# Kernel optimization log

Hardware: AMD Instinct MI355X
Metric: run time of the kernel (lower is better)

Reference implementation:

```python
import jax, jax.numpy as jnp
import numpy as np

RES = (512, 512)
NUM_CLASSES = 80
LEVELS = [(8, 0.0, 64.0), (16, 64.0, 128.0), (32, 128.0, 256.0),
          (64, 256.0, 512.0), (128, 512.0, jnp.inf)]


def _encode(boxes, labels, box_valid):
    """Vectorized FCOS encode. boxes:[B,N,4] (x1,y1,x2,y2), labels:[B,N] int,
    box_valid:[B,N] nonzero=valid. Returns 15 channel-first grids:
    (cls_P3..P7, centerness_P3..P7, ltrb_P3..P7)."""
    H, W = RES
    B, N, _ = boxes.shape
    valid = box_valid != 0
    x1, y1, x2, y2 = boxes[..., 0], boxes[..., 1], boxes[..., 2], boxes[..., 3]
    areas = (x2 - x1) * (y2 - y1)
    # sort descending by area (torch.sort descending); invalid boxes last
    order = jnp.argsort(-jnp.where(valid, areas, -jnp.inf), axis=1)  # [B,N]
    sb = jnp.take_along_axis(boxes, order[..., None], axis=1)        # [B,N,4]
    sl = jnp.take_along_axis(labels, order, axis=1)                  # [B,N]
    sv = jnp.take_along_axis(valid, order, axis=1)                   # [B,N]

    # initial per-level grids (NHWC during the scan, like the torch code)
    state = []
    for s, _, _ in LEVELS:
        Hl, Wl = H // s, W // s
        state.append((jnp.zeros((B, Hl, Wl, NUM_CLASSES), jnp.float32),
                      jnp.zeros((B, Hl, Wl, 1), jnp.float32),
                      jnp.zeros((B, Hl, Wl, 4), jnp.float32)))
    state = tuple(state)

    cls_ids = jnp.arange(NUM_CLASSES)

    def step(st, xs):
        box, lab, vld = xs  # [B,4], [B], [B]
        bxmin, bymin, bxmax, bymax = box[:, 0], box[:, 1], box[:, 2], box[:, 3]
        onehot = lab[:, None] == cls_ids[None, :]  # [B,C] bool
        new_st = []
        for li, (s, rmin, rmax) in enumerate(LEVELS):
            Hl, Wl = H // s, W // s
            # int() truncation as in torch _find_box_positions
            xf = jnp.trunc(bxmin / s + 0.5)
            xl = jnp.trunc(bxmax / s - 0.5)
            yf = jnp.trunc(bymin / s + 0.5)
            yl = jnp.trunc(bymax / s - 0.5)
            ys = jnp.arange(Hl, dtype=jnp.float32)
            xg = jnp.arange(Wl, dtype=jnp.float32)
            my = (ys[None, :] >= yf[:, None]) & (ys[None, :] <= yl[:, None])  # [B,Hl]
            mx = (xg[None, :] >= xf[:, None]) & (xg[None, :] <= xl[:, None])  # [B,Wl]
            mask = my[:, :, None] & mx[:, None, :] & vld[:, None, None]       # [B,Hl,Wl]
            cy = (ys + 0.5) * s  # [Hl]
            cx = (xg + 0.5) * s  # [Wl]
            l_ = jnp.broadcast_to(cx[None, None, :] - bxmin[:, None, None], (B, Hl, Wl))
            t_ = jnp.broadcast_to(cy[None, :, None] - bymin[:, None, None], (B, Hl, Wl))
            r_ = jnp.broadcast_to(bxmax[:, None, None] - cx[None, None, :], (B, Hl, Wl))
            b_ = jnp.broadcast_to(bymax[:, None, None] - cy[None, :, None], (B, Hl, Wl))
            ltrb = jnp.stack([l_, t_, r_, b_], axis=-1)  # [B,Hl,Wl,4]
            num = jnp.minimum(l_, r_) * jnp.minimum(t_, b_)
            den = jnp.maximum(l_, r_) * jnp.maximum(t_, b_)
            cent = jnp.sqrt(jnp.clip(num / jnp.maximum(den, 1e-12), 1e-12))
            mval = jnp.max(ltrb, axis=-1)
            cond = mask & (mval >= rmin) & (mval < rmax)  # [B,Hl,Wl]
            cls, cen, bx = st[li]
            cls = jnp.where(mask[..., None] & onehot[:, None, None, :],
                            cond[..., None].astype(cls.dtype), cls)
            cen = jnp.where(mask[..., None], cent[..., None], cen)
            bx = jnp.where(cond[..., None], ltrb, bx)
            new_st.append((cls, cen, bx))
        return tuple(new_st), None

    xs = (jnp.transpose(sb, (1, 0, 2)), jnp.transpose(sl, (1, 0)),
          jnp.transpose(sv, (1, 0)))
    state, _ = jax.lax.scan(step, state, xs)

    # channel-first like the torch permute at the end
    to_cf = lambda a: jnp.transpose(a, (0, 3, 1, 2))
    cls_out = tuple(to_cf(st[0]) for st in state)
    cen_out = tuple(to_cf(st[1]) for st in state)
    box_out = tuple(to_cf(st[2]) for st in state)
    return cls_out + cen_out + box_out


def setup_inputs() -> dict:
    key = jax.random.key(0)
    k1, k2, k3, k4 = jax.random.split(key, 4)
    B, N = 32, 100
    ctr = jax.random.uniform(k1, (B, N, 2), minval=16.0, maxval=496.0)
    wh = jax.random.uniform(k2, (B, N, 2), minval=8.0, maxval=300.0)
    mins = jnp.clip(ctr - wh / 2, 0.0, 511.0)
    maxs = jnp.clip(ctr + wh / 2, 0.0, 511.0)
    boxes = jnp.concatenate([mins, maxs], axis=-1)  # [B,N,4] x1,y1,x2,y2
    labels = jax.random.randint(k3, (B, N), 0, NUM_CLASSES)
    box_valid = jax.random.randint(k4, (B, N), 0, 2)
    return {"boxes": boxes, "labels": labels, "box_valid": box_valid}


def reference(boxes, labels, box_valid):
    return _encode(boxes, labels, box_valid)
```

## Files before the change

### kernel.cpp

```cpp
#include <hip/hip_runtime.h>
#include <math.h>

#define NBOX 100
#define NBATCH 32
#define NCLS 80
#define PIX_PER_BATCH 5456

__global__ __launch_bounds__(128) void fcos_sort_kernel(
    const float* __restrict__ boxes,
    const int* __restrict__ labels,
    const int* __restrict__ valid,
    float4* __restrict__ sboxes,
    int* __restrict__ slab)
{
    int b = blockIdx.x;
    int tid = threadIdx.x;
    __shared__ float area_s[NBOX];
    __shared__ float4 box_s[NBOX];
    __shared__ int lab_s[NBOX];
    if (tid < NBOX) {
        float4 bx = ((const float4*)boxes)[b * NBOX + tid];
        int v = valid[b * NBOX + tid];
        float area = (bx.z - bx.x) * (bx.w - bx.y);
        area_s[tid] = (v != 0) ? area : -INFINITY;
        box_s[tid] = bx;
        lab_s[tid] = (v != 0) ? labels[b * NBOX + tid] : -1;
    }
    __syncthreads();
    if (tid < NBOX) {
        float my = area_s[tid];
        int rank = 0;
        #pragma unroll 4
        for (int j = 0; j < NBOX; ++j) {
            float aj = area_s[j];
            rank += ((aj > my) || (aj == my && j < tid)) ? 1 : 0;
        }
        sboxes[b * NBOX + rank] = box_s[tid];
        slab[b * NBOX + rank] = lab_s[tid];
    }
}

__global__ __launch_bounds__(256) void fcos_encode_kernel(
    const float4* __restrict__ sboxes,
    const int* __restrict__ slab,
    float* __restrict__ out)
{
    __shared__ float4 sb[NBOX];
    __shared__ int sl[NBOX];
    int b = blockIdx.y;
    int tid = threadIdx.x;
    if (tid < NBOX) {
        sb[tid] = sboxes[b * NBOX + tid];
        sl[tid] = slab[b * NBOX + tid];
    }
    __syncthreads();

    int p = blockIdx.x * 256 + tid;
    if (p >= PIX_PER_BATCH) return;

    int base, lw;
    float s, rmin, rmax;
    int coff, ceoff, boff;
    if (p < 4096)       { base = 0;    lw = 6; s = 8.f;   rmin = 0.f;   rmax = 64.f;
                          coff = 0;        ceoff = 13967360; boff = 14141952; }
    else if (p < 5120)  { base = 4096; lw = 5; s = 16.f;  rmin = 64.f;  rmax = 128.f;
                          coff = 10485760; ceoff = 14098432; boff = 14666240; }
    else if (p < 5376)  { base = 5120; lw = 4; s = 32.f;  rmin = 128.f; rmax = 256.f;
                          coff = 13107200; ceoff = 14131200; boff = 14797312; }
    else if (p < 5440)  { base = 5376; lw = 3; s = 64.f;  rmin = 256.f; rmax = 512.f;
                          coff = 13762560; ceoff = 14139392; boff = 14830080; }
    else                { base = 5440; lw = 2; s = 128.f; rmin = 512.f; rmax = INFINITY;
                          coff = 13926400; ceoff = 14141440; boff = 14838272; }

    int rel = p - base;
    int W = 1 << lw;
    int A = W * W;
    int y = rel >> lw;
    int x = rel & (W - 1);

    float xF = (float)x, yF = (float)y;
    float cxp = (xF + 0.5f) * s;
    float cyp = (yF + 0.5f) * s;
    float inv_s = 1.0f / s;

    unsigned long long bits_lo = 0ull;
    unsigned int bits_hi = 0u;
    float cen = 0.f;
    float bl = 0.f, bt = 0.f, br = 0.f, bb = 0.f;

    for (int i = 0; i < NBOX; ++i) {
        int lab = sl[i];
        if (lab < 0) continue;
        float4 bx4 = sb[i];
        float xf = truncf(bx4.x * inv_s + 0.5f);
        float xl = truncf(bx4.z * inv_s - 0.5f);
        float yf = truncf(bx4.y * inv_s + 0.5f);
        float yl = truncf(bx4.w * inv_s - 0.5f);
        bool mask = (yF >= yf) & (yF <= yl) & (xF >= xf) & (xF <= xl);
        if (!mask) continue;

        float l_ = cxp - bx4.x;
        float t_ = cyp - bx4.y;
        float r_ = bx4.z - cxp;
        float b_ = bx4.w - cyp;
        float num = fminf(l_, r_) * fminf(t_, b_);
        float den = fmaxf(l_, r_) * fmaxf(t_, b_);
        cen = sqrtf(fmaxf(num / fmaxf(den, 1e-12f), 1e-12f));
        float mval = fmaxf(fmaxf(l_, t_), fmaxf(r_, b_));
        bool ok = (mval >= rmin) & (mval < rmax);

        if (lab < 64) {
            unsigned long long bit = 1ull << lab;
            bits_lo = ok ? (bits_lo | bit) : (bits_lo & ~bit);
        } else {
            unsigned int bit = 1u << (lab - 64);
            bits_hi = ok ? (bits_hi | bit) : (bits_hi & ~bit);
        }
        if (ok) { bl = l_; bt = t_; br = r_; bb = b_; }
    }

    {
        size_t o = (size_t)coff + (size_t)b * NCLS * A + rel;
        #pragma unroll 8
        for (int c = 0; c < 64; ++c) {
            out[o + (size_t)c * A] = ((bits_lo >> c) & 1ull) ? 1.0f : 0.0f;
        }
        #pragma unroll 8
        for (int c = 0; c < 16; ++c) {
            out[o + (size_t)(64 + c) * A] = ((bits_hi >> c) & 1u) ? 1.0f : 0.0f;
        }
    }
    out[(size_t)ceoff + (size_t)b * A + rel] = cen;
    {
        size_t o = (size_t)boff + (size_t)b * 4 * A + rel;
        out[o] = bl;
        out[o + (size_t)A] = bt;
        out[o + (size_t)2 * A] = br;
        out[o + (size_t)3 * A] = bb;
    }
}

extern "C" void kernel_launch(void* const* d_in, const int* in_sizes, int n_in,
                              void* d_out, int out_size, void* d_ws, size_t ws_size,
                              hipStream_t stream) {
    const float* boxes = (const float*)d_in[0];
    const int* labels = (const int*)d_in[1];
    const int* valid = (const int*)d_in[2];
    float* out = (float*)d_out;

    float4* sboxes = (float4*)d_ws;
    int* slab = (int*)((char*)d_ws + NBATCH * NBOX * sizeof(float4));

    fcos_sort_kernel<<<NBATCH, 128, 0, stream>>>(boxes, labels, valid, sboxes, slab);

    dim3 grid((PIX_PER_BATCH + 255) / 256, NBATCH);
    fcos_encode_kernel<<<grid, 256, 0, stream>>>(sboxes, slab, out);
}
```

Before: 99.67 us.

## Fuse sort into encode kernel and vectorize output stores via shared staging

Removes the separate sort kernel by having every encode block redo the per-batch rank sort in shared memory, saving a launch and the workspace round-trip. The per-box loop now breaks at the first invalid box, since invalid boxes sort last. Per-pixel results are staged in shared memory and written as float4 stores, with each wavefront covering a subset of class channels. The cost is redundant sorting in each block, extra shared memory, and a second barrier.

```diff
diff --git a/kernel.cpp b/kernel.cpp
--- a/kernel.cpp
+++ b/kernel.cpp
@@ -6,153 +6,174 @@
 #define NCLS 80
 #define PIX_PER_BATCH 5456
 
-__global__ __launch_bounds__(128) void fcos_sort_kernel(
-    const float* __restrict__ boxes,
+__device__ __forceinline__ void level_of(int p, int& base, int& lw, float& s,
+                                         float& rmin, float& rmax,
+                                         int& coff, int& ceoff, int& boff) {
+    if (p < 4096)      { base=0;    lw=6; s=8.f;   rmin=0.f;   rmax=64.f;
+                         coff=0;        ceoff=13967360; boff=14141952; }
+    else if (p < 5120) { base=4096; lw=5; s=16.f;  rmin=64.f;  rmax=128.f;
+                         coff=10485760; ceoff=14098432; boff=14666240; }
+    else if (p < 5376) { base=5120; lw=4; s=32.f;  rmin=128.f; rmax=256.f;
+                         coff=13107200; ceoff=14131200; boff=14797312; }
+    else if (p < 5440) { base=5376; lw=3; s=64.f;  rmin=256.f; rmax=512.f;
+                         coff=13762560; ceoff=14139392; boff=14830080; }
+    else               { base=5440; lw=2; s=128.f; rmin=512.f; rmax=INFINITY;
+                         coff=13926400; ceoff=14141440; boff=14838272; }
+}
+
+__global__ __launch_bounds__(256) void fcos_fused_kernel(
+    const float4* __restrict__ boxes,
     const int* __restrict__ labels,
     const int* __restrict__ valid,
-    float4* __restrict__ sboxes,
-    int* __restrict__ slab)
+    float* __restrict__ out)
 {
-    int b = blockIdx.x;
+    __shared__ float4 sbx[NBOX];
+    __shared__ int    slb[NBOX];
+    __shared__ float  sarea[NBOX];
+    __shared__ float4 rawb[NBOX];
+    __shared__ int    rawl[NBOX];
+    __shared__ unsigned w0s[256], w1s[256], w2s[256];
+    __shared__ float scen[256], slf[256], stf[256], srf[256], sbf[256];
+
+    int b = blockIdx.y;
     int tid = threadIdx.x;
-    __shared__ float area_s[NBOX];
-    __shared__ float4 box_s[NBOX];
-    __shared__ int lab_s[NBOX];
+
     if (tid < NBOX) {
-        float4 bx = ((const float4*)boxes)[b * NBOX + tid];
+        float4 bx = boxes[b * NBOX + tid];
         int v = valid[b * NBOX + tid];
-        float area = (bx.z - bx.x) * (bx.w - bx.y);
-        area_s[tid] = (v != 0) ? area : -INFINITY;
-        box_s[tid] = bx;
-        lab_s[tid] = (v != 0) ? labels[b * NBOX + tid] : -1;
+        rawb[tid] = bx;
+        sarea[tid] = (v != 0) ? (bx.z - bx.x) * (bx.w - bx.y) : -INFINITY;
+        rawl[tid] = (v != 0) ? labels[b * NBOX + tid] : -1;
     }
     __syncthreads();
     if (tid < NBOX) {
-        float my = area_s[tid];
+        float my = sarea[tid];
         int rank = 0;
         #pragma unroll 4
         for (int j = 0; j < NBOX; ++j) {
-            float aj = area_s[j];
+            float aj = sarea[j];
             rank += ((aj > my) || (aj == my && j < tid)) ? 1 : 0;
         }
-        sboxes[b * NBOX + rank] = box_s[tid];
-        slab[b * NBOX + rank] = lab_s[tid];
-    }
-}
-
-__global__ __launch_bounds__(256) void fcos_encode_kernel(
-    const float4* __restrict__ sboxes,
-    const int* __restrict__ slab,
-    float* __restrict__ out)
-{
-    __shared__ float4 sb[NBOX];
-    __shared__ int sl[NBOX];
-    int b = blockIdx.y;
-    int tid = threadIdx.x;
-    if (tid < NBOX) {
-        sb[tid] = sboxes[b * NBOX + tid];
-        sl[tid] = slab[b * NBOX + tid];
+        sbx[rank] = rawb[tid];
+        slb[rank] = rawl[tid];
     }
     __syncthreads();
 
     int p = blockIdx.x * 256 + tid;
-    if (p >= PIX_PER_BATCH) return;
+    unsigned long long bits_lo = 0ull;
+    unsigned bits_hi = 0u;
+    float cen = 0.f, bl = 0.f, bt = 0.f, br = 0.f, bb = 0.f;
 
-    int base, lw;
-    float s, rmin, rmax;
-    int coff, ceoff, boff;
-    if (p < 4096)       { base = 0;    lw = 6; s = 8.f;   rmin = 0.f;   rmax = 64.f;
-                          coff = 0;        ceoff = 13967360; boff = 14141952; }
-    else if (p < 5120)  { base = 4096; lw = 5; s = 16.f;  rmin = 64.f;  rmax = 128.f;
-                          coff = 10485760; ceoff = 14098432; boff = 14666240; }
-    else if (p < 5376)  { base = 5120; lw = 4; s = 32.f;  rmin = 128.f; rmax = 256.f;
-                          coff = 13107200; ceoff = 14131200; boff = 14797312; }
-    else if (p < 5440)  { base = 5376; lw = 3; s = 64.f;  rmin = 256.f; rmax = 512.f;
-                          coff = 13762560; ceoff = 14139392; boff = 14830080; }
-    else                { base = 5440; lw = 2; s = 128.f; rmin = 512.f; rmax = INFINITY;
-                          coff = 13926400; ceoff = 14141440; boff = 14838272; }
+    if (p < PIX_PER_BATCH) {
+        int base, lw, coff, ceoff, boff; float s, rmin, rmax;
+        level_of(p, base, lw, s, rmin, rmax, coff, ceoff, boff);
+        int rel = p - base;
+        int y = rel >> lw, x = rel & ((1 << lw) - 1);
+        float xF = (float)x, yF = (float)y;
+        float cxp = (xF + 0.5f) * s, cyp = (yF + 0.5f) * s;
+        float inv_s = 1.0f / s;
 
-    int rel = p - base;
-    int W = 1 << lw;
-    int A = W * W;
-    int y = rel >> lw;
-    int x = rel & (W - 1);
+        for (int i = 0; i < NBOX; ++i) {
+            int lab = slb[i];
+            if (lab < 0) break;
+            float4 bx4 = sbx[i];
+            float xf = truncf(bx4.x * inv_s + 0.5f);
+            float xl = truncf(bx4.z * inv_s - 0.5f);
+            float yf = truncf(bx4.y * inv_s + 0.5f);
+            float yl = truncf(bx4.w * inv_s - 0.5f);
+            bool mask = (yF >= yf) & (yF <= yl) & (xF >= xf) & (xF <= xl);
+            if (!mask) continue;
 
-    float xF = (float)x, yF = (float)y;
-    float cxp = (xF + 0.5f) * s;
-    float cyp = (yF + 0.5f) * s;
-    float inv_s = 1.0f / s;
+            float l_ = cxp - bx4.x;
+            float t_ = cyp - bx4.y;
+            float r_ = bx4.z - cxp;
+            float b_ = bx4.w - cyp;
+            float num = fminf(l_, r_) * fminf(t_, b_);
+            float den = fmaxf(l_, r_) * fmaxf(t_, b_);
+            cen = sqrtf(fmaxf(num / fmaxf(den, 1e-12f), 1e-12f));
+            float mval = fmaxf(fmaxf(l_, t_), fmaxf(r_, b_));
+            bool ok = (mval >= rmin) & (mval < rmax);
 
-    unsigned long long bits_lo = 0ull;
-    unsigned int bits_hi = 0u;
-    float cen = 0.f;
-    float bl = 0.f, bt = 0.f, br = 0.f, bb = 0.f;
-
-    for (int i = 0; i < NBOX; ++i) {
-        int lab = sl[i];
-        if (lab < 0) continue;
-        float4 bx4 = sb[i];
-        float xf = truncf(bx4.x * inv_s + 0.5f);
-        float xl = truncf(bx4.z * inv_s - 0.5f);
-        float yf = truncf(bx4.y * inv_s + 0.5f);
-        float yl = truncf(bx4.w * inv_s - 0.5f);
-        bool mask = (yF >= yf) & (yF <= yl) & (xF >= xf) & (xF <= xl);
-        if (!mask) continue;
-
-        float l_ = cxp - bx4.x;
-        float t_ = cyp - bx4.y;
-        float r_ = bx4.z - cxp;
-        float b_ = bx4.w - cyp;
-        float num = fminf(l_, r_) * fminf(t_, b_);
-        float den = fmaxf(l_, r_) * fmaxf(t_, b_);
-        cen = sqrtf(fmaxf(num / fmaxf(den, 1e-12f), 1e-12f));
-        float mval = fmaxf(fmaxf(l_, t_), fmaxf(r_, b_));
-        bool ok = (mval >= rmin) & (mval < rmax);
-
-        if (lab < 64) {
-            unsigned long long bit = 1ull << lab;
-            bits_lo = ok ? (bits_lo | bit) : (bits_lo & ~bit);
-        } else {
-            unsigned int bit = 1u << (lab - 64);
-            bits_hi = ok ? (bits_hi | bit) : (bits_hi & ~bit);
-        }
-        if (ok) { bl = l_; bt = t_; br = r_; bb = b_; }
-    }
-
-    {
-        size_t o = (size_t)coff + (size_t)b * NCLS * A + rel;
-        #pragma unroll 8
-        for (int c = 0; c < 64; ++c) {
-            out[o + (size_t)c * A] = ((bits_lo >> c) & 1ull) ? 1.0f : 0.0f;
-        }
-        #pragma unroll 8
-        for (int c = 0; c < 16; ++c) {
-            out[o + (size_t)(64 + c) * A] = ((bits_hi >> c) & 1u) ? 1.0f : 0.0f;
+            if (lab < 64) {
+                unsigned long long bit = 1ull << lab;
+                bits_lo = ok ? (bits_lo | bit) : (bits_lo & ~bit);
+            } else {
+                unsigned bit = 1u << (lab - 64);
+                bits_hi = ok ? (bits_hi | bit) : (bits_hi & ~bit);
+            }
+            if (ok) { bl = l_; bt = t_; br = r_; bb = b_; }
         }
     }
-    out[(size_t)ceoff + (size_t)b * A + rel] = cen;
-    {
-        size_t o = (size_t)boff + (size_t)b * 4 * A + rel;
-        out[o] = bl;
-        out[o + (size_t)A] = bt;
-        out[o + (size_t)2 * A] = br;
-        out[o + (size_t)3 * A] = bb;
+    w0s[tid] = (unsigned)bits_lo;
+    w1s[tid] = (unsigned)(bits_lo >> 32);
+    w2s[tid] = bits_hi;
+    scen[tid] = cen; slf[tid] = bl; stf[tid] = bt; srf[tid] = br; sbf[tid] = bb;
+    __syncthreads();
+
+    int lane = tid & 63, wv = tid >> 6;
+    int g = lane;
+    int gp = blockIdx.x * 256 + 4 * g;
+    if (gp < PIX_PER_BATCH) {
+        int base, lw, coff, ceoff, boff; float s, rmin, rmax;
+        level_of(gp, base, lw, s, rmin, rmax, coff, ceoff, boff);
+        int A = 1 << (2 * lw);
+        int relg = gp - base;
+
+        uint4 q0 = *(const uint4*)&w0s[4 * g];
+        uint4 q1 = *(const uint4*)&w1s[4 * g];
+        uint4 q2 = *(const uint4*)&w2s[4 * g];
+
+        size_t obase = (size_t)coff + (size_t)b * NCLS * A + relg;
+
+        #pragma unroll
+        for (int cc = 0; cc < 8; ++cc) {
+            int c = wv * 8 + cc;
+            float4 v;
+            v.x = ((q0.x >> c) & 1u) ? 1.f : 0.f;
+            v.y = ((q0.y >> c) & 1u) ? 1.f : 0.f;
+            v.z = ((q0.z >> c) & 1u) ? 1.f : 0.f;
+            v.w = ((q0.w >> c) & 1u) ? 1.f : 0.f;
+            *(float4*)&out[obase + (size_t)c * A] = v;
+        }
+        #pragma unroll
+        for (int cc = 0; cc < 8; ++cc) {
+            int c = wv * 8 + cc;
+            float4 v;
+            v.x = ((q1.x >> c) & 1u) ? 1.f : 0.f;
+            v.y = ((q1.y >> c) & 1u) ? 1.f : 0.f;
+            v.z = ((q1.z >> c) & 1u) ? 1.f : 0.f;
+            v.w = ((q1.w >> c) & 1u) ? 1.f : 0.f;
+            *(float4*)&out[obase + (size_t)(32 + c) * A] = v;
+        }
+        #pragma unroll
+        for (int cc = 0; cc < 4; ++cc) {
+            int c = wv * 4 + cc;
+            float4 v;
+            v.x = ((q2.x >> c) & 1u) ? 1.f : 0.f;
+            v.y = ((q2.y >> c) & 1u) ? 1.f : 0.f;
+            v.z = ((q2.z >> c) & 1u) ? 1.f : 0.f;
+            v.w = ((q2.w >> c) & 1u) ? 1.f : 0.f;
+            *(float4*)&out[obase + (size_t)(64 + c) * A] = v;
+        }
+
+        const float* barr = (wv == 0) ? slf : (wv == 1) ? stf : (wv == 2) ? srf : sbf;
+        float4 bv = *(const float4*)&barr[4 * g];
+        *(float4*)&out[(size_t)boff + (size_t)b * 4 * A + (size_t)wv * A + relg] = bv;
+        if (wv == 0) {
+            float4 cv = *(const float4*)&scen[4 * g];
+            *(float4*)&out[(size_t)ceoff + (size_t)b * A + relg] = cv;
+        }
     }
 }
 
 extern "C" void kernel_launch(void* const* d_in, const int* in_sizes, int n_in,
                               void* d_out, int out_size, void* d_ws, size_t ws_size,
                               hipStream_t stream) {
-    const float* boxes = (const float*)d_in[0];
+    const float4* boxes = (const float4*)d_in[0];
     const int* labels = (const int*)d_in[1];
     const int* valid = (const int*)d_in[2];
     float* out = (float*)d_out;
 
-    float4* sboxes = (float4*)d_ws;
-    int* slab = (int*)((char*)d_ws + NBATCH * NBOX * sizeof(float4));
-
-    fcos_sort_kernel<<<NBATCH, 128, 0, stream>>>(boxes, labels, valid, sboxes, slab);
-
     dim3 grid((PIX_PER_BATCH + 255) / 256, NBATCH);
-    fcos_encode_kernel<<<grid, 256, 0, stream>>>(sboxes, slab, out);
+    fcos_fused_kernel<<<grid, 256, 0, stream>>>(boxes, labels, valid, out);
 }
```

Measured after the change: 98.45 us. About the same (-1.2%).
